# Kernel tuning notes

Hardware: AMD Instinct MI355X
Metric: run time of the kernel (lower is better)

The kernel has to match this reference:

```python
import jax, jax.numpy as jnp
import numpy as np

B, S, D, H = 1, 4096, 512, 8
HD = D // H  # head_dims = 64


def setup_inputs() -> dict:
    key = jax.random.key(0)
    ks = jax.random.split(key, 12)
    scale = 0.02
    query = jax.random.normal(ks[0], (B, S, D), dtype=jnp.float32)
    key_t = jax.random.normal(ks[1], (B, S, D), dtype=jnp.float32)
    value = jax.random.normal(ks[2], (B, S, D), dtype=jnp.float32)
    mask = jax.random.randint(ks[3], (B, 1, S, S), 0, 2, dtype=jnp.int32)
    # per-head projection params (torch Linear: y = x @ W.T + b)
    Wq = jax.random.normal(ks[4], (HD, HD), dtype=jnp.float32) * scale
    bq = jax.random.normal(ks[5], (HD,), dtype=jnp.float32) * scale
    Wk = jax.random.normal(ks[6], (HD, HD), dtype=jnp.float32) * scale
    bk = jax.random.normal(ks[7], (HD,), dtype=jnp.float32) * scale
    Wv = jax.random.normal(ks[8], (HD, HD), dtype=jnp.float32) * scale
    bv = jax.random.normal(ks[9], (HD,), dtype=jnp.float32) * scale
    Wfc = jax.random.normal(ks[10], (D, D), dtype=jnp.float32) * scale
    bfc = jax.random.normal(ks[11], (D,), dtype=jnp.float32) * scale
    return {"query": query, "key": key_t, "value": value, "mask": mask,
            "Wq": Wq, "bq": bq, "Wk": Wk, "bk": bk, "Wv": Wv, "bv": bv,
            "Wfc": Wfc, "bfc": bfc}


def reference(query, key, value, mask, Wq, bq, Wk, bk, Wv, bv, Wfc, bfc):
    Batch, q_len, _ = query.shape
    k_len = key.shape[1]
    # reshape to [b, s, h, d] then apply per-head linear projections
    q = query.reshape(Batch, q_len, H, HD) @ Wq.T + bq
    k = key.reshape(Batch, k_len, H, HD) @ Wk.T + bk
    v = value.reshape(Batch, k_len, H, HD) @ Wv.T + bv
    # raw scores [b, h, q, k]; mask applied BEFORE scaling (as in original)
    score = jnp.einsum('bqhd,bkhd->bhqk', q, k)
    score = jnp.where(mask == 0, jnp.float32(-1e20), score)
    attn = jax.nn.softmax(score / jnp.sqrt(jnp.float32(HD)), axis=-1)
    out = jnp.einsum('bhqv,bvhd->bqhd', attn, v).reshape(Batch, q_len, D)
    return out @ Wfc.T + bfc
```

## Files before the change

### kernel.cpp

```cpp
#include <hip/hip_runtime.h>
#include <hip/hip_bf16.h>

#define S_LEN 4096
#define DMODEL 512
#define NHEAD 8
#define HDIM 64

typedef __bf16 bf16x8 __attribute__((ext_vector_type(8)));
typedef __bf16 bf16x4 __attribute__((ext_vector_type(4)));
typedef float f32x4 __attribute__((ext_vector_type(4)));

#define S2EXP 0.18033688011112042f

__device__ __forceinline__ void gload_lds16(const void* g, void* l) {
    __builtin_amdgcn_global_load_lds((const __attribute__((address_space(1))) void*)g,
                                     (__attribute__((address_space(3))) void*)l, 16, 0, 0);
}
__device__ __forceinline__ void gload_lds4(const void* g, void* l) {
    __builtin_amdgcn_global_load_lds((const __attribute__((address_space(1))) void*)g,
                                     (__attribute__((address_space(3))) void*)l, 4, 0, 0);
}

__global__ __launch_bounds__(256) void proj_all_kernel(const float* __restrict__ xq,
                                                       const float* __restrict__ xk,
                                                       const float* __restrict__ xv,
                                                       const float* __restrict__ Wq,
                                                       const float* __restrict__ bq,
                                                       const float* __restrict__ Wk,
                                                       const float* __restrict__ bk,
                                                       const float* __restrict__ Wv,
                                                       const float* __restrict__ bv,
                                                       __bf16* __restrict__ yq,
                                                       __bf16* __restrict__ yk,
                                                       __bf16* __restrict__ vt) {
    __shared__ float T[64][65];
    int bid = blockIdx.x;
    int t = threadIdx.x, wave = t >> 6, lane = t & 63, lg = lane >> 4, lc = lane & 15;
    if (bid < 512) {
        int r0 = bid * 64 + wave * 16;
        const float* xrq = xq + (size_t)(r0 + lc) * 64 + lg * 8;
        const float* xrk = xk + (size_t)(r0 + lc) * 64 + lg * 8;
        bf16x8 aq[2], ak[2];
#pragma unroll
        for (int c = 0; c < 2; ++c) {
            f32x4 u0 = *(const f32x4*)(xrq + c * 32);
            f32x4 u1 = *(const f32x4*)(xrq + c * 32 + 4);
            f32x4 v0 = *(const f32x4*)(xrk + c * 32);
            f32x4 v1 = *(const f32x4*)(xrk + c * 32 + 4);
            bf16x8 a, b;
#pragma unroll
            for (int j = 0; j < 4; ++j) {
                a[j] = (__bf16)u0[j]; a[4 + j] = (__bf16)u1[j];
                b[j] = (__bf16)v0[j]; b[4 + j] = (__bf16)v1[j];
            }
            aq[c] = a; ak[c] = b;
        }
#pragma unroll
        for (int nt = 0; nt < 4; ++nt) {
            const float* wq = Wq + (size_t)(nt * 16 + lc) * 64 + lg * 8;
            const float* wk = Wk + (size_t)(nt * 16 + lc) * 64 + lg * 8;
            f32x4 cq = {0, 0, 0, 0}, ck = {0, 0, 0, 0};
#pragma unroll
            for (int c = 0; c < 2; ++c) {
                f32x4 u0 = *(const f32x4*)(wq + c * 32);
                f32x4 u1 = *(const f32x4*)(wq + c * 32 + 4);
                f32x4 v0 = *(const f32x4*)(wk + c * 32);
                f32x4 v1 = *(const f32x4*)(wk + c * 32 + 4);
                bf16x8 bw, bw2;
#pragma unroll
                for (int j = 0; j < 4; ++j) {
                    bw[j] = (__bf16)u0[j]; bw[4 + j] = (__bf16)u1[j];
                    bw2[j] = (__bf16)v0[j]; bw2[4 + j] = (__bf16)v1[j];
                }
                cq = __builtin_amdgcn_mfma_f32_16x16x32_bf16(aq[c], bw, cq, 0, 0, 0);
                ck = __builtin_amdgcn_mfma_f32_16x16x32_bf16(ak[c], bw2, ck, 0, 0, 0);
            }
            float bqv = bq[nt * 16 + lc], bkv = bk[nt * 16 + lc];
#pragma unroll
            for (int r = 0; r < 4; ++r) {
                yq[(size_t)(r0 + lg * 4 + r) * 64 + nt * 16 + lc] = (__bf16)((cq[r] + bqv) * S2EXP);
                yk[(size_t)(r0 + lg * 4 + r) * 64 + nt * 16 + lc] = (__bf16)(ck[r] + bkv);
            }
        }
    } else {
        int vb = bid - 512;
        int h = vb & 7, s0 = (vb >> 3) * 64;
        const float* xr = xv + ((size_t)(s0 + wave * 16 + lc) * 8 + h) * 64 + lg * 8;
        bf16x8 av[2];
#pragma unroll
        for (int c = 0; c < 2; ++c) {
            f32x4 u0 = *(const f32x4*)(xr + c * 32);
            f32x4 u1 = *(const f32x4*)(xr + c * 32 + 4);
            bf16x8 a;
#pragma unroll
            for (int j = 0; j < 4; ++j) { a[j] = (__bf16)u0[j]; a[4 + j] = (__bf16)u1[j]; }
            av[c] = a;
        }
#pragma unroll
        for (int nt = 0; nt < 4; ++nt) {
            const float* wv = Wv + (size_t)(nt * 16 + lc) * 64 + lg * 8;
            f32x4 cv = {0, 0, 0, 0};
#pragma unroll
            for (int c = 0; c < 2; ++c) {
                f32x4 u0 = *(const f32x4*)(wv + c * 32);
                f32x4 u1 = *(const f32x4*)(wv + c * 32 + 4);
                bf16x8 bw;
#pragma unroll
                for (int j = 0; j < 4; ++j) { bw[j] = (__bf16)u0[j]; bw[4 + j] = (__bf16)u1[j]; }
                cv = __builtin_amdgcn_mfma_f32_16x16x32_bf16(av[c], bw, cv, 0, 0, 0);
            }
            float bvv = bv[nt * 16 + lc];
#pragma unroll
            for (int r = 0; r < 4; ++r) T[wave * 16 + lg * 4 + r][nt * 16 + lc] = cv[r] + bvv;
        }
        __syncthreads();
        int d = t >> 2, qr = t & 3;
        bf16x8 w0, w1;
#pragma unroll
        for (int i = 0; i < 8; ++i) {
            w0[i] = (__bf16)T[qr * 16 + i][d];
            w1[i] = (__bf16)T[qr * 16 + 8 + i][d];
        }
        __bf16* dst = vt + ((size_t)h * 64 + d) * 4096 + s0 + qr * 16;
        *(bf16x8*)(dst) = w0;
        *(bf16x8*)(dst + 8) = w1;
    }
}

__global__ __launch_bounds__(256) void prep_kernel(const int* __restrict__ mask,
                                                   unsigned int* __restrict__ pack,
                                                   const float* __restrict__ Wfc,
                                                   __bf16* __restrict__ wfc_bf) {
    int bid = blockIdx.x;
    int t = threadIdx.x;
    if (bid < 2048) {
        int lane = t & 63;
        int wid = bid * 4 + (t >> 6);
#pragma unroll 4
        for (int it = 0; it < 32; ++it) {
            int gw = wid * 32 + it;
            int qi = gw >> 6, seg = gw & 63;
            unsigned long long bits = __ballot(mask[(size_t)qi * 4096 + seg * 64 + lane] != 0);
            if (lane == 0)
                *(unsigned long long*)(&pack[(size_t)qi * 128 + seg * 2]) = bits;
        }
    } else {
        int b = bid - 2048;
        const f32x4* s4 = (const f32x4*)Wfc;
#pragma unroll
        for (int i = 0; i < 8; ++i) {
            int idx = (b * 8 + i) * 256 + t;
            f32x4 v = s4[idx];
            bf16x4 o;
#pragma unroll
            for (int j = 0; j < 4; ++j) o[j] = (__bf16)v[j];
            *(bf16x4*)(wfc_bf + (size_t)idx * 4) = o;
        }
    }
}

__global__ __launch_bounds__(256, 3) void attn_kernel(const __bf16* __restrict__ qb,
                                                      const __bf16* __restrict__ kb,
                                                      const __bf16* __restrict__ vt,
                                                      const unsigned int* __restrict__ mp,
                                                      int split_steps,
                                                      float* __restrict__ opart,
                                                      float* __restrict__ stats,
                                                      __bf16* __restrict__ ao) {
    int bid = blockIdx.x;
    int h = bid & 7, qtb = (bid >> 3) & 31, sp = bid >> 8;
    int kv0 = sp * split_steps * 32;
    int nsteps = min(split_steps, 128 - sp * split_steps);
    int t = threadIdx.x, wave = t >> 6, lane = t & 63, lg = lane >> 4, lc = lane & 15;
    int q0 = qtb * 128 + wave * 32;

    __shared__ __bf16 Kt[4][32 * 64];
    __shared__ __bf16 Vt[4][64 * 32];
    __shared__ __bf16 P[4][32 * 32];
    __shared__ unsigned int Mld[4][128];

    int srK = lane >> 3;
    int cgK = (lane & 7) ^ srK;
    int srV = lane >> 2;
    int cgV = ((lane & 3) - ((lane >> 3) & 3)) & 3;

    const __bf16* qr0 = qb + ((size_t)(q0 + lc) * 8 + h) * 64 + lg * 8;
    const __bf16* qr1 = qb + ((size_t)(q0 + 16 + lc) * 8 + h) * 64 + lg * 8;
    bf16x8 qf00 = *(const bf16x8*)(qr0);
    bf16x8 qf01 = *(const bf16x8*)(qr0 + 32);
    bf16x8 qf10 = *(const bf16x8*)(qr1);
    bf16x8 qf11 = *(const bf16x8*)(qr1 + 32);

    bf16x8 onesf;
#pragma unroll
    for (int j = 0; j < 8; ++j) onesf[j] = (__bf16)1.0f;

    f32x4 o00 = {0,0,0,0}, o01 = {0,0,0,0}, o02 = {0,0,0,0}, o03 = {0,0,0,0};
    f32x4 o10 = {0,0,0,0}, o11 = {0,0,0,0}, o12 = {0,0,0,0}, o13 = {0,0,0,0};
    f32x4 lac0 = {0,0,0,0}, lac1 = {0,0,0,0};

    const __bf16* vbase = vt + (size_t)h * 64 * 4096;
    const unsigned int* mbase = mp + (size_t)(qtb * 128 + wave * 64 + lane) * 128 + (kv0 >> 5);

    int rotP = (lc >> 1) & 3;
    int lg4 = lg * 4;

#define STAGE(tt, B)                                                                          \
    {                                                                                         \
        if (wave < 2) gload_lds4(mbase + (tt), &Mld[B][wave * 64]);                           \
        gload_lds16(kb + (size_t)(kv0 + (tt) * 32 + wave * 8 + srK) * 512 + h * 64 + cgK * 8, \
                    &Kt[B][wave * 512]);                                                      \
        gload_lds16(vbase + (size_t)(wave * 16 + srV) * 4096 + kv0 + (tt) * 32 + cgV * 8,     \
                    &Vt[B][wave * 512]);                                                      \
    }

    STAGE(0, 0)
    STAGE(1, 1)
    asm volatile("s_waitcnt vmcnt(0)" ::: "memory");
    __builtin_amdgcn_s_barrier();

#define ATTN_STEP(s, C, G)                                                                    \
    {                                                                                         \
        STAGE(min((s) + 2, nsteps - 1), G)                                                    \
        asm volatile("s_waitcnt vmcnt(4)" ::: "memory");                                      \
        __builtin_amdgcn_s_barrier();                                                         \
        unsigned int mw0 = Mld[C][wave * 32 + lc] >> lg4;                                     \
        unsigned int mw1 = Mld[C][wave * 32 + 16 + lc] >> lg4;                                \
        const char* Kb = (const char*)&Kt[C][0];                                              \
        f32x4 s00 = {0,0,0,0}, s01 = {0,0,0,0}, s10 = {0,0,0,0}, s11 = {0,0,0,0};             \
        {                                                                                     \
            int row = lc, sw = (row & 7) << 4;                                                \
            bf16x8 ka = *(const bf16x8*)(Kb + ((row * 128 + lg * 16) ^ sw));                  \
            bf16x8 kc_ = *(const bf16x8*)(Kb + ((row * 128 + 64 + lg * 16) ^ sw));            \
            s00 = __builtin_amdgcn_mfma_f32_16x16x32_bf16(ka, qf00, s00, 0, 0, 0);            \
            s00 = __builtin_amdgcn_mfma_f32_16x16x32_bf16(kc_, qf01, s00, 0, 0, 0);           \
            s01 = __builtin_amdgcn_mfma_f32_16x16x32_bf16(ka, qf10, s01, 0, 0, 0);            \
            s01 = __builtin_amdgcn_mfma_f32_16x16x32_bf16(kc_, qf11, s01, 0, 0, 0);           \
        }                                                                                     \
        {                                                                                     \
            int row = 16 + lc, sw = (row & 7) << 4;                                           \
            bf16x8 ka = *(const bf16x8*)(Kb + ((row * 128 + lg * 16) ^ sw));                  \
            bf16x8 kc_ = *(const bf16x8*)(Kb + ((row * 128 + 64 + lg * 16) ^ sw));            \
            s10 = __builtin_amdgcn_mfma_f32_16x16x32_bf16(ka, qf00, s10, 0, 0, 0);            \
            s10 = __builtin_amdgcn_mfma_f32_16x16x32_bf16(kc_, qf01, s10, 0, 0, 0);           \
            s11 = __builtin_amdgcn_mfma_f32_16x16x32_bf16(ka, qf10, s11, 0, 0, 0);            \
            s11 = __builtin_amdgcn_mfma_f32_16x16x32_bf16(kc_, qf11, s11, 0, 0, 0);           \
        }                                                                                     \
        char* pb = (char*)&P[wave][0];                                                        \
        {                                                                                     \
            bf16x4 k0q0, k1q0, k0q1, k1q1;                                                    \
            _Pragma("unroll")                                                                 \
            for (int r = 0; r < 4; ++r) {                                                     \
                float pa = __builtin_amdgcn_exp2f(s00[r]);                                    \
                k0q0[r] = (__bf16)__int_as_float(__float_as_int(pa) &                         \
                                                 __builtin_amdgcn_sbfe((int)mw0, r, 1));      \
                float pc = __builtin_amdgcn_exp2f(s10[r]);                                    \
                k1q0[r] = (__bf16)__int_as_float(__float_as_int(pc) &                         \
                                                 __builtin_amdgcn_sbfe((int)mw0, 16 + r, 1)); \
                float pd = __builtin_amdgcn_exp2f(s01[r]);                                    \
                k0q1[r] = (__bf16)__int_as_float(__float_as_int(pd) &                         \
                                                 __builtin_amdgcn_sbfe((int)mw1, r, 1));      \
                float pe = __builtin_amdgcn_exp2f(s11[r]);                                    \
                k1q1[r] = (__bf16)__int_as_float(__float_as_int(pe) &                         \
                                                 __builtin_amdgcn_sbfe((int)mw1, 16 + r, 1)); \
            }                                                                                 \
            int ph0 = ((lg >> 1) + rotP) & 3;                                                 \
            int ph1 = (2 + (lg >> 1) + rotP) & 3;                                             \
            int ib = (lg & 1) * 8;                                                            \
            *(bf16x4*)(pb + lc * 64 + ph0 * 16 + ib) = k0q0;                                  \
            *(bf16x4*)(pb + lc * 64 + ph1 * 16 + ib) = k1q0;                                  \
            *(bf16x4*)(pb + 1024 + lc * 64 + ph0 * 16 + ib) = k0q1;                           \
            *(bf16x4*)(pb + 1024 + lc * 64 + ph1 * 16 + ib) = k1q1;                           \
        }                                                                                     \
        int prd = lc * 64 + (((lg + rotP) & 3) * 16);                                         \
        bf16x8 pf0 = *(const bf16x8*)(pb + prd);                                              \
        bf16x8 pf1 = *(const bf16x8*)(pb + 1024 + prd);                                       \
        lac0 = __builtin_amdgcn_mfma_f32_16x16x32_bf16(pf0, onesf, lac0, 0, 0, 0);            \
        lac1 = __builtin_amdgcn_mfma_f32_16x16x32_bf16(pf1, onesf, lac1, 0, 0, 0);            \
        const char* Vb = (const char*)&Vt[C][0];                                              \
        {                                                                                     \
            bf16x8 vf = *(const bf16x8*)(Vb + ((0 * 16 + lc) * 64 + (((lg + rotP) & 3) * 16)));\
            o00 = __builtin_amdgcn_mfma_f32_16x16x32_bf16(pf0, vf, o00, 0, 0, 0);             \
            o10 = __builtin_amdgcn_mfma_f32_16x16x32_bf16(pf1, vf, o10, 0, 0, 0);             \
        }                                                                                     \
        {                                                                                     \
            bf16x8 vf = *(const bf16x8*)(Vb + ((1 * 16 + lc) * 64 + (((lg + rotP) & 3) * 16)));\
            o01 = __builtin_amdgcn_mfma_f32_16x16x32_bf16(pf0, vf, o01, 0, 0, 0);             \
            o11 = __builtin_amdgcn_mfma_f32_16x16x32_bf16(pf1, vf, o11, 0, 0, 0);             \
        }                                                                                     \
        {                                                                                     \
            bf16x8 vf = *(const bf16x8*)(Vb + ((2 * 16 + lc) * 64 + (((lg + rotP) & 3) * 16)));\
            o02 = __builtin_amdgcn_mfma_f32_16x16x32_bf16(pf0, vf, o02, 0, 0, 0);             \
            o12 = __builtin_amdgcn_mfma_f32_16x16x32_bf16(pf1, vf, o12, 0, 0, 0);             \
        }                                                                                     \
        {                                                                                     \
            bf16x8 vf = *(const bf16x8*)(Vb + ((3 * 16 + lc) * 64 + (((lg + rotP) & 3) * 16)));\
            o03 = __builtin_amdgcn_mfma_f32_16x16x32_bf16(pf0, vf, o03, 0, 0, 0);             \
            o13 = __builtin_amdgcn_mfma_f32_16x16x32_bf16(pf1, vf, o13, 0, 0, 0);             \
        }                                                                                     \
    }

    int s = 0;
    for (; s + 4 <= nsteps; s += 4) {
        ATTN_STEP(s + 0, 0, 2)
        ATTN_STEP(s + 1, 1, 3)
        ATTN_STEP(s + 2, 2, 0)
        ATTN_STEP(s + 3, 3, 1)
    }
    if (s < nsteps) { ATTN_STEP(s, 0, 2) s++; }
    if (s < nsteps) { ATTN_STEP(s, 1, 3) s++; }
    if (s < nsteps) { ATTN_STEP(s, 2, 0) s++; }
#undef ATTN_STEP
#undef STAGE

    if (opart) {
        if (lc == 0) {
#pragma unroll
            for (int r = 0; r < 4; ++r) {
                stats[(size_t)sp * 32768 + (size_t)(q0 + lg * 4 + r) * 8 + h]      = lac0[r];
                stats[(size_t)sp * 32768 + (size_t)(q0 + 16 + lg * 4 + r) * 8 + h] = lac1[r];
            }
        }
#pragma unroll
        for (int r = 0; r < 4; ++r) {
            size_t rh0 = (size_t)sp * 32768 + (size_t)(q0 + lg * 4 + r) * 8 + h;
            float* d0 = opart + rh0 * 64;
            d0[0 * 16 + lc] = o00[r]; d0[1 * 16 + lc] = o01[r];
            d0[2 * 16 + lc] = o02[r]; d0[3 * 16 + lc] = o03[r];
            size_t rh1 = (size_t)sp * 32768 + (size_t)(q0 + 16 + lg * 4 + r) * 8 + h;
            float* d1 = opart + rh1 * 64;
            d1[0 * 16 + lc] = o10[r]; d1[1 * 16 + lc] = o11[r];
            d1[2 * 16 + lc] = o12[r]; d1[3 * 16 + lc] = o13[r];
        }
    } else {
#pragma unroll
        for (int r = 0; r < 4; ++r) {
            float inv0 = 1.0f / lac0[r];
            __bf16* d0 = ao + (size_t)(q0 + lg * 4 + r) * 512 + h * 64;
            d0[0 * 16 + lc] = (__bf16)(o00[r] * inv0); d0[1 * 16 + lc] = (__bf16)(o01[r] * inv0);
            d0[2 * 16 + lc] = (__bf16)(o02[r] * inv0); d0[3 * 16 + lc] = (__bf16)(o03[r] * inv0);
            float inv1 = 1.0f / lac1[r];
            __bf16* d1 = ao + (size_t)(q0 + 16 + lg * 4 + r) * 512 + h * 64;
            d1[0 * 16 + lc] = (__bf16)(o10[r] * inv1); d1[1 * 16 + lc] = (__bf16)(o11[r] * inv1);
            d1[2 * 16 + lc] = (__bf16)(o12[r] * inv1); d1[3 * 16 + lc] = (__bf16)(o13[r] * inv1);
        }
    }
}

__global__ __launch_bounds__(256) void combine_kernel(const float* __restrict__ opart,
                                                      const float* __restrict__ stats,
                                                      __bf16* __restrict__ ao, int nsplit) {
    int t = threadIdx.x, lane = t & 63, w = t >> 6;
    int rh = blockIdx.x * 4 + w;
    float L = 0.f, acc = 0.f;
#pragma unroll 3
    for (int sp = 0; sp < nsplit; ++sp) {
        L += stats[(size_t)sp * 32768 + rh];
        acc += opart[((size_t)sp * 32768 + rh) * 64 + lane];
    }
    int row = rh >> 3, h = rh & 7;
    ao[(size_t)row * 512 + h * 64 + lane] = (__bf16)(acc / L);
}

__global__ __launch_bounds__(256) void fc_kernel(const __bf16* __restrict__ ao,
                                                 const __bf16* __restrict__ Wb,
                                                 const float* __restrict__ bfc,
                                                 float* __restrict__ out) {
    int bid = blockIdx.x;
    int stile = bid >> 3, nt = bid & 7;
    int t = threadIdx.x, wave = t >> 6, lane = t & 63, lg = lane >> 4, lc = lane & 15;
    int s0 = stile * 64 + wave * 16;
    int n0 = nt * 64;
    f32x4 c0 = {0,0,0,0}, c1 = {0,0,0,0}, c2 = {0,0,0,0}, c3 = {0,0,0,0};
    for (int k0 = 0; k0 < 512; k0 += 32) {
        bf16x8 af = *(const bf16x8*)(ao + (size_t)(s0 + lc) * 512 + k0 + lg * 8);
        const __bf16* wb = Wb + k0 + lg * 8;
        c0 = __builtin_amdgcn_mfma_f32_16x16x32_bf16(af, *(const bf16x8*)(wb + (size_t)(n0 + 0 * 16 + lc) * 512), c0, 0, 0, 0);
        c1 = __builtin_amdgcn_mfma_f32_16x16x32_bf16(af, *(const bf16x8*)(wb + (size_t)(n0 + 1 * 16 + lc) * 512), c1, 0, 0, 0);
        c2 = __builtin_amdgcn_mfma_f32_16x16x32_bf16(af, *(const bf16x8*)(wb + (size_t)(n0 + 2 * 16 + lc) * 512), c2, 0, 0, 0);
        c3 = __builtin_amdgcn_mfma_f32_16x16x32_bf16(af, *(const bf16x8*)(wb + (size_t)(n0 + 3 * 16 + lc) * 512), c3, 0, 0, 0);
    }
#pragma unroll
    for (int r = 0; r < 4; ++r) {
        int row = s0 + lg * 4 + r;
        float* dst = out + (size_t)row * 512 + n0;
        dst[0 * 16 + lc] = c0[r] + bfc[n0 + 0 * 16 + lc];
        dst[1 * 16 + lc] = c1[r] + bfc[n0 + 1 * 16 + lc];
        dst[2 * 16 + lc] = c2[r] + bfc[n0 + 2 * 16 + lc];
        dst[3 * 16 + lc] = c3[r] + bfc[n0 + 3 * 16 + lc];
    }
}

extern "C" void kernel_launch(void* const* d_in, const int* in_sizes, int n_in,
                              void* d_out, int out_size, void* d_ws, size_t ws_size,
                              hipStream_t stream) {
    const float* query = (const float*)d_in[0];
    const float* key   = (const float*)d_in[1];
    const float* value = (const float*)d_in[2];
    const int*   mask  = (const int*)d_in[3];
    const float* Wq  = (const float*)d_in[4];
    const float* bq  = (const float*)d_in[5];
    const float* Wk  = (const float*)d_in[6];
    const float* bk  = (const float*)d_in[7];
    const float* Wv  = (const float*)d_in[8];
    const float* bv  = (const float*)d_in[9];
    const float* Wfc = (const float*)d_in[10];
    const float* bfc = (const float*)d_in[11];

    char* ws = (char*)d_ws;
    const size_t MB = 1024 * 1024;
    __bf16* q_bf   = (__bf16*)(ws + 0 * MB);
    __bf16* k_bf   = (__bf16*)(ws + 4 * MB);
    __bf16* vt     = (__bf16*)(ws + 8 * MB);
    __bf16* ao     = (__bf16*)(ws + 12 * MB);
    __bf16* wfc_bf = (__bf16*)(ws + 16 * MB);
    unsigned int* mpack = (unsigned int*)(ws + 17 * MB);
    const size_t base = 19 * MB;
    int nsplit = (ws_size >= base + 3 * (8 * MB) + 3 * 131072) ? 3 : 1;
    float* opart = (float*)(ws + base);
    float* stats = (float*)(ws + base + (size_t)nsplit * 8 * MB);

    proj_all_kernel<<<1024, 256, 0, stream>>>(query, key, value, Wq, bq, Wk, bk, Wv, bv,
                                              q_bf, k_bf, vt);
    prep_kernel<<<2080, 256, 0, stream>>>(mask, mpack, Wfc, wfc_bf);
    if (nsplit > 1) {
        attn_kernel<<<256 * nsplit, 256, 0, stream>>>(q_bf, k_bf, vt, mpack,
                                                      43, opart, stats, ao);
        combine_kernel<<<8192, 256, 0, stream>>>(opart, stats, ao, nsplit);
    } else {
        attn_kernel<<<256, 256, 0, stream>>>(q_bf, k_bf, vt, mpack,
                                             128, nullptr, nullptr, ao);
    }
    fc_kernel<<<512, 256, 0, stream>>>(ao, wfc_bf, bfc, (float*)d_out);
}
```

Baseline: 119.6 us.

## Feed P from registers via 16x16x16 MFMA, drop LDS P round-trip, split KV four ways

Replaces the per-step LDS store and reload of the probability tile with direct register use. It switches the PV and row-sum products to the 16x16x16 bf16 MFMA, whose operand layout matches the S accumulator layout, and transposes the output accumulator orientation so stores become vectorized. It also changes the KV split from 3 ways of 43 steps to 4 ways of 32 steps (or 2 ways), removing the tail handling, and raises the occupancy hint to 4 blocks per CU. This trades the LDS traffic and barriers for twice as many smaller MFMA instructions, plus extra partial-sum traffic in the combine pass.

```diff
diff --git a/kernel.cpp b/kernel.cpp
--- a/kernel.cpp
+++ b/kernel.cpp
@@ -8,6 +8,7 @@
 
 typedef __bf16 bf16x8 __attribute__((ext_vector_type(8)));
 typedef __bf16 bf16x4 __attribute__((ext_vector_type(4)));
+typedef short s16x4 __attribute__((ext_vector_type(4)));
 typedef float f32x4 __attribute__((ext_vector_type(4)));
 
 #define S2EXP 0.18033688011112042f
@@ -19,6 +20,10 @@
 __device__ __forceinline__ void gload_lds4(const void* g, void* l) {
     __builtin_amdgcn_global_load_lds((const __attribute__((address_space(1))) void*)g,
                                      (__attribute__((address_space(3))) void*)l, 4, 0, 0);
+}
+__device__ __forceinline__ f32x4 mfma16(bf16x4 a, bf16x4 b, f32x4 c) {
+    return __builtin_amdgcn_mfma_f32_16x16x16bf16_1k(__builtin_bit_cast(s16x4, a),
+                                                     __builtin_bit_cast(s16x4, b), c, 0, 0, 0);
 }
 
 __global__ __launch_bounds__(256) void proj_all_kernel(const float* __restrict__ xq,
@@ -159,7 +164,7 @@
     }
 }
 
-__global__ __launch_bounds__(256, 3) void attn_kernel(const __bf16* __restrict__ qb,
+__global__ __launch_bounds__(256, 4) void attn_kernel(const __bf16* __restrict__ qb,
                                                       const __bf16* __restrict__ kb,
                                                       const __bf16* __restrict__ vt,
                                                       const unsigned int* __restrict__ mp,
@@ -170,19 +175,18 @@
     int bid = blockIdx.x;
     int h = bid & 7, qtb = (bid >> 3) & 31, sp = bid >> 8;
     int kv0 = sp * split_steps * 32;
-    int nsteps = min(split_steps, 128 - sp * split_steps);
+    int nsteps = split_steps;
     int t = threadIdx.x, wave = t >> 6, lane = t & 63, lg = lane >> 4, lc = lane & 15;
     int q0 = qtb * 128 + wave * 32;
 
     __shared__ __bf16 Kt[4][32 * 64];
     __shared__ __bf16 Vt[4][64 * 32];
-    __shared__ __bf16 P[4][32 * 32];
     __shared__ unsigned int Mld[4][128];
 
     int srK = lane >> 3;
     int cgK = (lane & 7) ^ srK;
+    int cgV = ((lane & 3) - ((lane >> 3) & 3)) & 3;
     int srV = lane >> 2;
-    int cgV = ((lane & 3) - ((lane >> 3) & 3)) & 3;
 
     const __bf16* qr0 = qb + ((size_t)(q0 + lc) * 8 + h) * 64 + lg * 8;
     const __bf16* qr1 = qb + ((size_t)(q0 + 16 + lc) * 8 + h) * 64 + lg * 8;
@@ -191,9 +195,9 @@
     bf16x8 qf10 = *(const bf16x8*)(qr1);
     bf16x8 qf11 = *(const bf16x8*)(qr1 + 32);
 
-    bf16x8 onesf;
-#pragma unroll
-    for (int j = 0; j < 8; ++j) onesf[j] = (__bf16)1.0f;
+    bf16x4 onesA;
+#pragma unroll
+    for (int j = 0; j < 4; ++j) onesA[j] = (__bf16)1.0f;
 
     f32x4 o00 = {0,0,0,0}, o01 = {0,0,0,0}, o02 = {0,0,0,0}, o03 = {0,0,0,0};
     f32x4 o10 = {0,0,0,0}, o11 = {0,0,0,0}, o12 = {0,0,0,0}, o13 = {0,0,0,0};
@@ -202,8 +206,9 @@
     const __bf16* vbase = vt + (size_t)h * 64 * 4096;
     const unsigned int* mbase = mp + (size_t)(qtb * 128 + wave * 64 + lane) * 128 + (kv0 >> 5);
 
-    int rotP = (lc >> 1) & 3;
     int lg4 = lg * 4;
+    int vch0 = ((((lg >> 1) + (lc >> 1)) & 3) * 16) + (lg & 1) * 8;
+    int vch1 = (((2 + (lg >> 1) + (lc >> 1)) & 3) * 16) + (lg & 1) * 8;
 
 #define STAGE(tt, B)                                                                          \
     {                                                                                         \
@@ -246,104 +251,109 @@
             s11 = __builtin_amdgcn_mfma_f32_16x16x32_bf16(ka, qf10, s11, 0, 0, 0);            \
             s11 = __builtin_amdgcn_mfma_f32_16x16x32_bf16(kc_, qf11, s11, 0, 0, 0);           \
         }                                                                                     \
-        char* pb = (char*)&P[wave][0];                                                        \
-        {                                                                                     \
-            bf16x4 k0q0, k1q0, k0q1, k1q1;                                                    \
-            _Pragma("unroll")                                                                 \
-            for (int r = 0; r < 4; ++r) {                                                     \
-                float pa = __builtin_amdgcn_exp2f(s00[r]);                                    \
-                k0q0[r] = (__bf16)__int_as_float(__float_as_int(pa) &                         \
-                                                 __builtin_amdgcn_sbfe((int)mw0, r, 1));      \
-                float pc = __builtin_amdgcn_exp2f(s10[r]);                                    \
-                k1q0[r] = (__bf16)__int_as_float(__float_as_int(pc) &                         \
-                                                 __builtin_amdgcn_sbfe((int)mw0, 16 + r, 1)); \
-                float pd = __builtin_amdgcn_exp2f(s01[r]);                                    \
-                k0q1[r] = (__bf16)__int_as_float(__float_as_int(pd) &                         \
-                                                 __builtin_amdgcn_sbfe((int)mw1, r, 1));      \
-                float pe = __builtin_amdgcn_exp2f(s11[r]);                                    \
-                k1q1[r] = (__bf16)__int_as_float(__float_as_int(pe) &                         \
-                                                 __builtin_amdgcn_sbfe((int)mw1, 16 + r, 1)); \
-            }                                                                                 \
-            int ph0 = ((lg >> 1) + rotP) & 3;                                                 \
-            int ph1 = (2 + (lg >> 1) + rotP) & 3;                                             \
-            int ib = (lg & 1) * 8;                                                            \
-            *(bf16x4*)(pb + lc * 64 + ph0 * 16 + ib) = k0q0;                                  \
-            *(bf16x4*)(pb + lc * 64 + ph1 * 16 + ib) = k1q0;                                  \
-            *(bf16x4*)(pb + 1024 + lc * 64 + ph0 * 16 + ib) = k0q1;                           \
-            *(bf16x4*)(pb + 1024 + lc * 64 + ph1 * 16 + ib) = k1q1;                           \
-        }                                                                                     \
-        int prd = lc * 64 + (((lg + rotP) & 3) * 16);                                         \
-        bf16x8 pf0 = *(const bf16x8*)(pb + prd);                                              \
-        bf16x8 pf1 = *(const bf16x8*)(pb + 1024 + prd);                                       \
-        lac0 = __builtin_amdgcn_mfma_f32_16x16x32_bf16(pf0, onesf, lac0, 0, 0, 0);            \
-        lac1 = __builtin_amdgcn_mfma_f32_16x16x32_bf16(pf1, onesf, lac1, 0, 0, 0);            \
+        bf16x4 pk00, pk10, pk01, pk11;                                        \
+        _Pragma("unroll")                                                                     \
+        for (int r = 0; r < 4; ++r) {                                                         \
+            float pa = __builtin_amdgcn_exp2f(s00[r]);                                        \
+            pk00[r] = (__bf16)__int_as_float(__float_as_int(pa) &                             \
+                                             __builtin_amdgcn_sbfe((int)mw0, r, 1));          \
+            float pc = __builtin_amdgcn_exp2f(s10[r]);                                        \
+            pk10[r] = (__bf16)__int_as_float(__float_as_int(pc) &                             \
+                                             __builtin_amdgcn_sbfe((int)mw0, 16 + r, 1));     \
+            float pd = __builtin_amdgcn_exp2f(s01[r]);                                        \
+            pk01[r] = (__bf16)__int_as_float(__float_as_int(pd) &                             \
+                                             __builtin_amdgcn_sbfe((int)mw1, r, 1));          \
+            float pe = __builtin_amdgcn_exp2f(s11[r]);                                        \
+            pk11[r] = (__bf16)__int_as_float(__float_as_int(pe) &                             \
+                                             __builtin_amdgcn_sbfe((int)mw1, 16 + r, 1));     \
+        }                                                                                     \
+        lac0 = mfma16(onesA, pk00, lac0);                                                     \
+        lac0 = mfma16(onesA, pk10, lac0);                                                     \
+        lac1 = mfma16(onesA, pk01, lac1);                                                     \
+        lac1 = mfma16(onesA, pk11, lac1);                                                     \
         const char* Vb = (const char*)&Vt[C][0];                                              \
         {                                                                                     \
-            bf16x8 vf = *(const bf16x8*)(Vb + ((0 * 16 + lc) * 64 + (((lg + rotP) & 3) * 16)));\
-            o00 = __builtin_amdgcn_mfma_f32_16x16x32_bf16(pf0, vf, o00, 0, 0, 0);             \
-            o10 = __builtin_amdgcn_mfma_f32_16x16x32_bf16(pf1, vf, o10, 0, 0, 0);             \
-        }                                                                                     \
-        {                                                                                     \
-            bf16x8 vf = *(const bf16x8*)(Vb + ((1 * 16 + lc) * 64 + (((lg + rotP) & 3) * 16)));\
-            o01 = __builtin_amdgcn_mfma_f32_16x16x32_bf16(pf0, vf, o01, 0, 0, 0);             \
-            o11 = __builtin_amdgcn_mfma_f32_16x16x32_bf16(pf1, vf, o11, 0, 0, 0);             \
-        }                                                                                     \
-        {                                                                                     \
-            bf16x8 vf = *(const bf16x8*)(Vb + ((2 * 16 + lc) * 64 + (((lg + rotP) & 3) * 16)));\
-            o02 = __builtin_amdgcn_mfma_f32_16x16x32_bf16(pf0, vf, o02, 0, 0, 0);             \
-            o12 = __builtin_amdgcn_mfma_f32_16x16x32_bf16(pf1, vf, o12, 0, 0, 0);             \
-        }                                                                                     \
-        {                                                                                     \
-            bf16x8 vf = *(const bf16x8*)(Vb + ((3 * 16 + lc) * 64 + (((lg + rotP) & 3) * 16)));\
-            o03 = __builtin_amdgcn_mfma_f32_16x16x32_bf16(pf0, vf, o03, 0, 0, 0);             \
-            o13 = __builtin_amdgcn_mfma_f32_16x16x32_bf16(pf1, vf, o13, 0, 0, 0);             \
-        }                                                                                     \
-    }
-
-    int s = 0;
-    for (; s + 4 <= nsteps; s += 4) {
+            int rb = (0 * 16 + lc) * 64;                                                      \
+            bf16x4 v0 = *(const bf16x4*)(Vb + rb + vch0);                                     \
+            bf16x4 v1 = *(const bf16x4*)(Vb + rb + vch1);                                     \
+            o00 = mfma16(v0, pk00, o00); o00 = mfma16(v1, pk10, o00);                         \
+            o10 = mfma16(v0, pk01, o10); o10 = mfma16(v1, pk11, o10);                         \
+        }                                                                                     \
+        {                                                                                     \
+            int rb = (1 * 16 + lc) * 64;                                                      \
+            bf16x4 v0 = *(const bf16x4*)(Vb + rb + vch0);                                     \
+            bf16x4 v1 = *(const bf16x4*)(Vb + rb + vch1);                                     \
+            o01 = mfma16(v0, pk00, o01); o01 = mfma16(v1, pk10, o01);                         \
+            o11 = mfma16(v0, pk01, o11); o11 = mfma16(v1, pk11, o11);                         \
+        }                                                                                     \
+        {                                                                                     \
+            int rb = (2 * 16 + lc) * 64;                                                      \
+            bf16x4 v0 = *(const bf16x4*)(Vb + rb + vch0);                                     \
+            bf16x4 v1 = *(const bf16x4*)(Vb + rb + vch1);                                     \
+            o02 = mfma16(v0, pk00, o02); o02 = mfma16(v1, pk10, o02);                         \
+            o12 = mfma16(v0, pk01, o12); o12 = mfma16(v1, pk11, o12);                         \
+        }                                                                                     \
+        {                                                                                     \
+            int rb = (3 * 16 + lc) * 64;                                                      \
+            bf16x4 v0 = *(const bf16x4*)(Vb + rb + vch0);                                     \
+            bf16x4 v1 = *(const bf16x4*)(Vb + rb + vch1);                                     \
+            o03 = mfma16(v0, pk00, o03); o03 = mfma16(v1, pk10, o03);                         \
+            o13 = mfma16(v0, pk01, o13); o13 = mfma16(v1, pk11, o13);                         \
+        }                                                                                     \
+    }
+
+    for (int s = 0; s < nsteps; s += 4) {
         ATTN_STEP(s + 0, 0, 2)
         ATTN_STEP(s + 1, 1, 3)
         ATTN_STEP(s + 2, 2, 0)
         ATTN_STEP(s + 3, 3, 1)
     }
-    if (s < nsteps) { ATTN_STEP(s, 0, 2) s++; }
-    if (s < nsteps) { ATTN_STEP(s, 1, 3) s++; }
-    if (s < nsteps) { ATTN_STEP(s, 2, 0) s++; }
 #undef ATTN_STEP
 #undef STAGE
 
     if (opart) {
-        if (lc == 0) {
-#pragma unroll
-            for (int r = 0; r < 4; ++r) {
-                stats[(size_t)sp * 32768 + (size_t)(q0 + lg * 4 + r) * 8 + h]      = lac0[r];
-                stats[(size_t)sp * 32768 + (size_t)(q0 + 16 + lg * 4 + r) * 8 + h] = lac1[r];
-            }
-        }
-#pragma unroll
-        for (int r = 0; r < 4; ++r) {
-            size_t rh0 = (size_t)sp * 32768 + (size_t)(q0 + lg * 4 + r) * 8 + h;
-            float* d0 = opart + rh0 * 64;
-            d0[0 * 16 + lc] = o00[r]; d0[1 * 16 + lc] = o01[r];
-            d0[2 * 16 + lc] = o02[r]; d0[3 * 16 + lc] = o03[r];
-            size_t rh1 = (size_t)sp * 32768 + (size_t)(q0 + 16 + lg * 4 + r) * 8 + h;
-            float* d1 = opart + rh1 * 64;
-            d1[0 * 16 + lc] = o10[r]; d1[1 * 16 + lc] = o11[r];
-            d1[2 * 16 + lc] = o12[r]; d1[3 * 16 + lc] = o13[r];
-        }
+        if (lg == 0) {
+            stats[(size_t)sp * 32768 + (size_t)(q0 + lc) * 8 + h]      = lac0[0];
+            stats[(size_t)sp * 32768 + (size_t)(q0 + 16 + lc) * 8 + h] = lac1[0];
+        }
+        size_t rh0 = (size_t)sp * 32768 + (size_t)(q0 + lc) * 8 + h;
+        size_t rh1 = (size_t)sp * 32768 + (size_t)(q0 + 16 + lc) * 8 + h;
+        float* d0 = opart + rh0 * 64 + lg4;
+        float* d1 = opart + rh1 * 64 + lg4;
+        *(f32x4*)(d0 + 0)  = o00; *(f32x4*)(d0 + 16) = o01;
+        *(f32x4*)(d0 + 32) = o02; *(f32x4*)(d0 + 48) = o03;
+        *(f32x4*)(d1 + 0)  = o10; *(f32x4*)(d1 + 16) = o11;
+        *(f32x4*)(d1 + 32) = o12; *(f32x4*)(d1 + 48) = o13;
     } else {
-#pragma unroll
-        for (int r = 0; r < 4; ++r) {
-            float inv0 = 1.0f / lac0[r];
-            __bf16* d0 = ao + (size_t)(q0 + lg * 4 + r) * 512 + h * 64;
-            d0[0 * 16 + lc] = (__bf16)(o00[r] * inv0); d0[1 * 16 + lc] = (__bf16)(o01[r] * inv0);
-            d0[2 * 16 + lc] = (__bf16)(o02[r] * inv0); d0[3 * 16 + lc] = (__bf16)(o03[r] * inv0);
-            float inv1 = 1.0f / lac1[r];
-            __bf16* d1 = ao + (size_t)(q0 + 16 + lg * 4 + r) * 512 + h * 64;
-            d1[0 * 16 + lc] = (__bf16)(o10[r] * inv1); d1[1 * 16 + lc] = (__bf16)(o11[r] * inv1);
-            d1[2 * 16 + lc] = (__bf16)(o12[r] * inv1); d1[3 * 16 + lc] = (__bf16)(o13[r] * inv1);
-        }
+        float inv0 = 1.0f / lac0[0];
+        float inv1 = 1.0f / lac1[0];
+        __bf16* d0 = ao + (size_t)(q0 + lc) * 512 + h * 64 + lg4;
+        __bf16* d1 = ao + (size_t)(q0 + 16 + lc) * 512 + h * 64 + lg4;
+        bf16x4 w;
+#pragma unroll
+        for (int r = 0; r < 4; ++r) w[r] = (__bf16)(o00[r] * inv0);
+        *(bf16x4*)(d0 + 0) = w;
+#pragma unroll
+        for (int r = 0; r < 4; ++r) w[r] = (__bf16)(o01[r] * inv0);
+        *(bf16x4*)(d0 + 16) = w;
+#pragma unroll
+        for (int r = 0; r < 4; ++r) w[r] = (__bf16)(o02[r] * inv0);
+        *(bf16x4*)(d0 + 32) = w;
+#pragma unroll
+        for (int r = 0; r < 4; ++r) w[r] = (__bf16)(o03[r] * inv0);
+        *(bf16x4*)(d0 + 48) = w;
+#pragma unroll
+        for (int r = 0; r < 4; ++r) w[r] = (__bf16)(o10[r] * inv1);
+        *(bf16x4*)(d1 + 0) = w;
+#pragma unroll
+        for (int r = 0; r < 4; ++r) w[r] = (__bf16)(o11[r] * inv1);
+        *(bf16x4*)(d1 + 16) = w;
+#pragma unroll
+        for (int r = 0; r < 4; ++r) w[r] = (__bf16)(o12[r] * inv1);
+        *(bf16x4*)(d1 + 32) = w;
+#pragma unroll
+        for (int r = 0; r < 4; ++r) w[r] = (__bf16)(o13[r] * inv1);
+        *(bf16x4*)(d1 + 48) = w;
     }
 }
 
@@ -353,7 +363,7 @@
     int t = threadIdx.x, lane = t & 63, w = t >> 6;
     int rh = blockIdx.x * 4 + w;
     float L = 0.f, acc = 0.f;
-#pragma unroll 3
+#pragma unroll 4
     for (int sp = 0; sp < nsplit; ++sp) {
         L += stats[(size_t)sp * 32768 + rh];
         acc += opart[((size_t)sp * 32768 + rh) * 64 + lane];
@@ -416,7 +426,9 @@
     __bf16* wfc_bf = (__bf16*)(ws + 16 * MB);
     unsigned int* mpack = (unsigned int*)(ws + 17 * MB);
     const size_t base = 19 * MB;
-    int nsplit = (ws_size >= base + 3 * (8 * MB) + 3 * 131072) ? 3 : 1;
+    int nsplit = 1, split_steps = 128;
+    if (ws_size >= base + 4 * (8 * MB) + 4 * 131072)      { nsplit = 4; split_steps = 32; }
+    else if (ws_size >= base + 2 * (8 * MB) + 2 * 131072) { nsplit = 2; split_steps = 64; }
     float* opart = (float*)(ws + base);
     float* stats = (float*)(ws + base + (size_t)nsplit * 8 * MB);
 
@@ -425,7 +437,7 @@
     prep_kernel<<<2080, 256, 0, stream>>>(mask, mpack, Wfc, wfc_bf);
     if (nsplit > 1) {
         attn_kernel<<<256 * nsplit, 256, 0, stream>>>(q_bf, k_bf, vt, mpack,
-                                                      43, opart, stats, ao);
+                                                      split_steps, opart, stats, ao);
         combine_kernel<<<8192, 256, 0, stream>>>(opart, stats, ao, nsplit);
     } else {
         attn_kernel<<<256, 256, 0, stream>>>(q_bf, k_bf, vt, mpack,
```

After: 123.3 us. +3.1%, slower.
